# Kernel tuning notes

Hardware: AMD Instinct MI355X
Metric: run time of the kernel (lower is better)

## Reference

```python
import jax, jax.numpy as jnp
import numpy as np

EPS = 1e-7  # keras.backend.epsilon()
NUM_ROUTING = 3


def squash(v, axis=-1):
    s2 = jnp.sum(jnp.square(v), axis=axis, keepdims=True)
    scale = s2 / (1.0 + s2) / jnp.sqrt(s2 + EPS)
    return scale * v


def setup_inputs() -> dict:
    key = jax.random.key(0)
    k1, k2 = jax.random.split(key)
    B, N_in, C, d_in, d_out = 64, 4096, 10, 8, 16
    x = jax.random.normal(k1, (B, N_in, d_in), dtype=jnp.float32)
    # glorot-ish scale for transformation weights [N_in, C, d_in, d_out]
    W = jax.random.normal(k2, (N_in, C, d_in, d_out), dtype=jnp.float32) * (1.0 / np.sqrt(d_in + d_out))
    return {"x": x, "W": W}


def reference(x, W):
    # u_hat[b,n,c,e] = sum_d x[b,n,d] * W[n,c,d,e]  -- the tile+multiply+reduce in the original
    u_hat = jnp.einsum('bnd,ncde->bnce', x, W)  # [B, N_in, C, d_out]
    B, N_in, C, _ = u_hat.shape
    b = jnp.zeros((B, N_in, C), dtype=u_hat.dtype)
    v = None
    for i in range(NUM_ROUTING):
        c = jax.nn.softmax(b, axis=2)                    # [B, N_in, C]
        s = jnp.einsum('bnc,bnce->bce', c, u_hat)        # [B, C, d_out]
        v = squash(s)                                    # [B, C, d_out]
        if i < NUM_ROUTING - 1:
            agreement = jnp.einsum('bnce,bce->bnc', u_hat, v)
            b = b + agreement
    return v
```

## Files before the change

kernel.cpp:

```cpp
#include <hip/hip_runtime.h>
#include <hip/hip_fp16.h>

#define B_ 64
#define N_ 4096
#define C_ 10
#define D_ 8
#define E_ 16
#define EPS_ 1e-7f
#define NT_ 4
#define NBLK_ (N_ / NT_)
#define NSLOT_ NBLK_
#define PROW_ 80
#define NSG_ 8

typedef _Float16 h2_t __attribute__((ext_vector_type(2)));
typedef __fp16   p2_t __attribute__((ext_vector_type(2)));

__device__ inline unsigned pkh(float a, float b) {
    p2_t t = __builtin_amdgcn_cvt_pkrtz(a, b);
    return *(unsigned*)&t;
}
#if __has_builtin(__builtin_amdgcn_fdot2)
__device__ inline float fd2(unsigned a, unsigned b, float c) {
    h2_t av = *(h2_t*)&a, bv = *(h2_t*)&b;
    return __builtin_amdgcn_fdot2(av, bv, c, false);
}
#else
__device__ inline float fd2(unsigned a, unsigned b, float c) {
    h2_t av = *(h2_t*)&a, bv = *(h2_t*)&b;
    return fmaf((float)av.x, (float)bv.x, fmaf((float)av.y, (float)bv.y, c));
}
#endif
__device__ inline float hlo(unsigned u) { h2_t t = *(h2_t*)&u; return (float)t.x; }
__device__ inline float hhi(unsigned u) { h2_t t = *(h2_t*)&u; return (float)t.y; }
__device__ inline unsigned hpack(float a, float b) {
    __half2 t = __floats2half2_rn(a, b);
    return *(unsigned*)&t;
}
__device__ inline float2 hunpack(unsigned u) {
    return __half22float2(*(const __half2*)&u);
}

template <bool UNIFORM>
__global__ __launch_bounds__(256, 4) void caps_pass(
    const float* __restrict__ x, const float* __restrict__ W,
    const unsigned* __restrict__ vpk, unsigned* __restrict__ partial)
{
    __shared__ uint4    wlds[NT_ * C_ * 16];
    __shared__ unsigned xlds[NT_ * B_ * 4];
    __shared__ float    xch[2][2][2][16][2];

    const int tid = (int)threadIdx.x;
    const int blk = (int)blockIdx.x;
    const int n0  = blk * NT_;

    {
        const float4* wg = (const float4*)W + (size_t)blk * (NT_ * 320);
#pragma unroll
        for (int k = 0; k < 3; ++k) {
            const int g = k * 256 + tid;
            if (g < NT_ * C_ * 16) {
                const int n   = g / 160;
                const int rem = g - n * 160;
                const int c   = rem >> 4;
                const int r2  = rem & 15;
                const int d2  = r2 >> 2;
                const int eqs = r2 & 3;
                const float4 g0 = wg[n * 320 + c * 32 + (2 * d2) * 4 + eqs];
                const float4 g1 = wg[n * 320 + c * 32 + (2 * d2 + 1) * 4 + eqs];
                wlds[((n * C_ + c) * 4 + d2) * 4 + eqs] =
                    make_uint4(pkh(g0.x, g1.x), pkh(g0.y, g1.y),
                               pkh(g0.z, g1.z), pkh(g0.w, g1.w));
            }
        }
    }
    {
        const float4* xg = (const float4*)x;
#pragma unroll
        for (int k = 0; k < 2; ++k) {
            const int g = k * 256 + tid;
            const int b = g >> 3;
            const int r = g & 7;
            const int n = r >> 1;
            const int dq = r & 1;
            const float4 v = xg[((size_t)b * N_ + n0 + n) * 2 + dq];
            *(uint2*)&xlds[(n * B_ + b) * 4 + dq * 2] =
                make_uint2(pkh(v.x, v.y), pkh(v.z, v.w));
        }
    }
    __syncthreads();

    const int wv   = tid >> 6;
    const int lane = tid & 63;
    const int eq   = lane & 3;
    const int bl   = lane >> 2;
    const int h    = wv & 1;
    const int cg   = wv >> 1;
    const int b0   = h * 32 + bl;
    const int b1   = b0 + 16;
    const int cbase = cg * 5;

    unsigned vcp0[5][2], vcp1[5][2];
    if (!UNIFORM) {
#pragma unroll
        for (int cc = 0; cc < 5; ++cc) {
            const int c = cbase + cc;
            const uint2 a = *(const uint2*)(vpk + (b0 * C_ + c) * 8 + eq * 2);
            vcp0[cc][0] = a.x; vcp0[cc][1] = a.y;
            const uint2 d = *(const uint2*)(vpk + (b1 * C_ + c) * 8 + eq * 2);
            vcp1[cc][0] = d.x; vcp1[cc][1] = d.y;
        }
    }

    float4 acc0[5], acc1[5];
#pragma unroll
    for (int cc = 0; cc < 5; ++cc) {
        acc0[cc] = make_float4(0.f, 0.f, 0.f, 0.f);
        acc1[cc] = make_float4(0.f, 0.f, 0.f, 0.f);
    }

#pragma unroll 1
    for (int j = 0; j < NT_; ++j) {
        const uint4 xq0 = *(const uint4*)&xlds[(j * B_ + b0) * 4];
        const uint4 xq1 = *(const uint4*)&xlds[(j * B_ + b1) * 4];
        const unsigned xa[4] = {xq0.x, xq0.y, xq0.z, xq0.w};
        const unsigned xb[4] = {xq1.x, xq1.y, xq1.z, xq1.w};

        if (UNIFORM) {
#pragma unroll
            for (int cc = 0; cc < 5; ++cc) {
                const uint4* wq = &wlds[(j * C_ + cbase + cc) * 16];
#pragma unroll
                for (int d2 = 0; d2 < 4; ++d2) {
                    const uint4 q = wq[d2 * 4 + eq];
                    acc0[cc].x = fd2(xa[d2], q.x, acc0[cc].x);
                    acc0[cc].y = fd2(xa[d2], q.y, acc0[cc].y);
                    acc0[cc].z = fd2(xa[d2], q.z, acc0[cc].z);
                    acc0[cc].w = fd2(xa[d2], q.w, acc0[cc].w);
                    acc1[cc].x = fd2(xb[d2], q.x, acc1[cc].x);
                    acc1[cc].y = fd2(xb[d2], q.y, acc1[cc].y);
                    acc1[cc].z = fd2(xb[d2], q.z, acc1[cc].z);
                    acc1[cc].w = fd2(xb[d2], q.w, acc1[cc].w);
                }
            }
        } else {
            unsigned uhp0[5][2], uhp1[5][2];
            float wgt0[5], wgt1[5];
            float s0 = 0.f, s1 = 0.f;
#pragma unroll
            for (int cc = 0; cc < 5; ++cc) {
                const uint4* wq = &wlds[(j * C_ + cbase + cc) * 16];
                float4 u0 = make_float4(0.f, 0.f, 0.f, 0.f);
                float4 u1 = make_float4(0.f, 0.f, 0.f, 0.f);
#pragma unroll
                for (int d2 = 0; d2 < 4; ++d2) {
                    const uint4 q = wq[d2 * 4 + eq];
                    u0.x = fd2(xa[d2], q.x, u0.x);
                    u0.y = fd2(xa[d2], q.y, u0.y);
                    u0.z = fd2(xa[d2], q.z, u0.z);
                    u0.w = fd2(xa[d2], q.w, u0.w);
                    u1.x = fd2(xb[d2], q.x, u1.x);
                    u1.y = fd2(xb[d2], q.y, u1.y);
                    u1.z = fd2(xb[d2], q.z, u1.z);
                    u1.w = fd2(xb[d2], q.w, u1.w);
                }
                const unsigned up00 = pkh(u0.x, u0.y), up01 = pkh(u0.z, u0.w);
                const unsigned up10 = pkh(u1.x, u1.y), up11 = pkh(u1.z, u1.w);
                float t0 = fd2(up00, vcp0[cc][0], fd2(up01, vcp0[cc][1], 0.f));
                t0 += __shfl_xor(t0, 1); t0 += __shfl_xor(t0, 2);
                float t1 = fd2(up10, vcp1[cc][0], fd2(up11, vcp1[cc][1], 0.f));
                t1 += __shfl_xor(t1, 1); t1 += __shfl_xor(t1, 2);
                wgt0[cc] = __expf(t0); s0 += wgt0[cc];
                wgt1[cc] = __expf(t1); s1 += wgt1[cc];
                uhp0[cc][0] = up00; uhp0[cc][1] = up01;
                uhp1[cc][0] = up10; uhp1[cc][1] = up11;
            }
            if (eq == 0) {
                xch[j & 1][cg][h][bl][0] = s0;
                xch[j & 1][cg][h][bl][1] = s1;
            }
            __syncthreads();
            const float i0 = 1.f / (s0 + xch[j & 1][cg ^ 1][h][bl][0]);
            const float i1 = 1.f / (s1 + xch[j & 1][cg ^ 1][h][bl][1]);
#pragma unroll
            for (int cc = 0; cc < 5; ++cc) {
                const float g0 = wgt0[cc] * i0, g1 = wgt1[cc] * i1;
                acc0[cc].x = fmaf(g0, hlo(uhp0[cc][0]), acc0[cc].x);
                acc0[cc].y = fmaf(g0, hhi(uhp0[cc][0]), acc0[cc].y);
                acc0[cc].z = fmaf(g0, hlo(uhp0[cc][1]), acc0[cc].z);
                acc0[cc].w = fmaf(g0, hhi(uhp0[cc][1]), acc0[cc].w);
                acc1[cc].x = fmaf(g1, hlo(uhp1[cc][0]), acc1[cc].x);
                acc1[cc].y = fmaf(g1, hhi(uhp1[cc][0]), acc1[cc].y);
                acc1[cc].z = fmaf(g1, hlo(uhp1[cc][1]), acc1[cc].z);
                acc1[cc].w = fmaf(g1, hhi(uhp1[cc][1]), acc1[cc].w);
            }
        }
    }

    const float fold = UNIFORM ? 0.1f : 1.f;
#pragma unroll
    for (int cc = 0; cc < 5; ++cc) {
        const int c = cbase + cc;
        *(uint2*)(partial + ((size_t)b0 * NSLOT_ + blk) * PROW_ + c * 8 + eq * 2) =
            make_uint2(hpack(acc0[cc].x * fold, acc0[cc].y * fold),
                       hpack(acc0[cc].z * fold, acc0[cc].w * fold));
        *(uint2*)(partial + ((size_t)b1 * NSLOT_ + blk) * PROW_ + c * 8 + eq * 2) =
            make_uint2(hpack(acc1[cc].x * fold, acc1[cc].y * fold),
                       hpack(acc1[cc].z * fold, acc1[cc].w * fold));
    }
}

__global__ __launch_bounds__(256) void caps_redA(
    const unsigned* __restrict__ partial, float* __restrict__ sub)
{
    const int b  = (int)blockIdx.x >> 3;
    const int sg = (int)blockIdx.x & 7;
    const int tid = (int)threadIdx.x;
    const int sc   = tid >> 5;
    const int col4 = tid & 31;
    __shared__ float red[8][20][8];
    if (col4 < 20) {
        float s[8];
#pragma unroll
        for (int p = 0; p < 8; ++p) s[p] = 0.f;
        const int slot0 = sg * (NSLOT_ / NSG_) + sc * 16;
        const uint4* base = (const uint4*)(partial +
            ((size_t)b * NSLOT_ + slot0) * PROW_) + col4;
#pragma unroll 4
        for (int k = 0; k < 16; ++k) {
            const uint4 q = base[k * (PROW_ / 4)];
            const float2 f0 = hunpack(q.x), f1 = hunpack(q.y);
            const float2 f2 = hunpack(q.z), f3 = hunpack(q.w);
            s[0] += f0.x; s[1] += f0.y; s[2] += f1.x; s[3] += f1.y;
            s[4] += f2.x; s[5] += f2.y; s[6] += f3.x; s[7] += f3.y;
        }
#pragma unroll
        for (int p = 0; p < 8; ++p) red[sc][col4][p] = s[p];
    }
    __syncthreads();
    if (tid < 160) {
        const int c4 = tid >> 3, p = tid & 7;
        float s = 0.f;
#pragma unroll
        for (int ch = 0; ch < 8; ++ch) s += red[ch][c4][p];
        sub[((size_t)b * NSG_ + sg) * (C_ * E_) + c4 * 8 + p] = s;
    }
}

__global__ __launch_bounds__(128) void caps_redB(
    const float* __restrict__ sub, float* __restrict__ v_cum,
    unsigned* __restrict__ vpk, float* __restrict__ out, int mode)
{
    const int b = (int)blockIdx.x;
    const int tid = (int)threadIdx.x;
    if (tid >= PROW_) return;
    float slo = 0.f, shi = 0.f;
#pragma unroll
    for (int sg = 0; sg < NSG_; ++sg) {
        const float* p = sub + ((size_t)b * NSG_ + sg) * (C_ * E_) + tid * 2;
        slo += p[0]; shi += p[1];
    }
    float p = slo * slo + shi * shi;
    p += __shfl_xor(p, 1); p += __shfl_xor(p, 2); p += __shfl_xor(p, 4);
    const float sc = (p / (1.f + p)) * rsqrtf(p + EPS_);
    float v0 = sc * slo, v1 = sc * shi;
    const int o = b * (C_ * E_) + tid * 2;
    if (mode == 2) {
        out[o] = v0; out[o + 1] = v1;
    } else {
        if (mode == 0) {
            v_cum[o] = v0; v_cum[o + 1] = v1;
        } else {
            v0 += v_cum[o]; v1 += v_cum[o + 1];
            v_cum[o] = v0; v_cum[o + 1] = v1;
        }
        vpk[b * PROW_ + tid] = hpack(v0, v1);
    }
}

extern "C" void kernel_launch(void* const* d_in, const int* in_sizes, int n_in,
                              void* d_out, int out_size, void* d_ws, size_t ws_size,
                              hipStream_t stream) {
    const float* x = (const float*)d_in[0];
    const float* W = (const float*)d_in[1];
    float* out = (float*)d_out;

    char* p = (char*)d_ws;
    unsigned* partial = (unsigned*)p;
    p += (size_t)B_ * NSLOT_ * PROW_ * sizeof(unsigned);
    float* sub = (float*)p;
    p += (size_t)B_ * NSG_ * C_ * E_ * sizeof(float);
    float* v_cum = (float*)p;
    p += (size_t)B_ * C_ * E_ * sizeof(float);
    unsigned* vpk = (unsigned*)p;

    for (int t = 0; t < 3; ++t) {
        if (t == 0)
            caps_pass<true ><<<dim3(NBLK_), 256, 0, stream>>>(x, W, vpk, partial);
        else
            caps_pass<false><<<dim3(NBLK_), 256, 0, stream>>>(x, W, vpk, partial);
        caps_redA<<<dim3(B_ * NSG_), 256, 0, stream>>>(partial, sub);
        caps_redB<<<dim3(B_), 128, 0, stream>>>(sub, v_cum, vpk, out, t);
    }
}
```

Before: 82.87 us.

## Process eight input capsules per block with in-block pairwise reduction of partials

Doubles the capsules handled per block (NT 4→8) and uses 512 threads, so two groups of waves each take four capsules and their fp16 partial sums are combined through shared memory before one global write. This halves the partial buffer size and the number of slots the reduction kernel has to read. In exchange it adds an extra shared-memory round trip and barriers, halves the block count, and makes blocks larger, which may reduce occupancy.

```diff
diff --git a/kernel.cpp b/kernel.cpp
--- a/kernel.cpp
+++ b/kernel.cpp
@@ -7,10 +7,11 @@
 #define D_ 8
 #define E_ 16
 #define EPS_ 1e-7f
-#define NT_ 4
+#define NT_ 8
 #define NBLK_ (N_ / NT_)
 #define NSLOT_ NBLK_
 #define PROW_ 80
+#define WBROW_ 82
 #define NSG_ 8
 
 typedef _Float16 h2_t __attribute__((ext_vector_type(2)));
@@ -42,13 +43,15 @@
 }
 
 template <bool UNIFORM>
-__global__ __launch_bounds__(256, 4) void caps_pass(
+__global__ __launch_bounds__(512, 4) void caps_pass(
     const float* __restrict__ x, const float* __restrict__ W,
     const unsigned* __restrict__ vpk, unsigned* __restrict__ partial)
 {
-    __shared__ uint4    wlds[NT_ * C_ * 16];
-    __shared__ unsigned xlds[NT_ * B_ * 4];
-    __shared__ float    xch[2][2][2][16][2];
+    __shared__ __align__(16) char smem[30720];
+    uint4*    wlds = (uint4*)smem;
+    unsigned* xlds = (unsigned*)(smem + 20480);
+    float*    xch  = (float*)(smem + 28672);
+    unsigned* wb   = (unsigned*)smem;
 
     const int tid = (int)threadIdx.x;
     const int blk = (int)blockIdx.x;
@@ -58,7 +61,7 @@
         const float4* wg = (const float4*)W + (size_t)blk * (NT_ * 320);
 #pragma unroll
         for (int k = 0; k < 3; ++k) {
-            const int g = k * 256 + tid;
+            const int g = k * 512 + tid;
             if (g < NT_ * C_ * 16) {
                 const int n   = g / 160;
                 const int rem = g - n * 160;
@@ -78,9 +81,9 @@
         const float4* xg = (const float4*)x;
 #pragma unroll
         for (int k = 0; k < 2; ++k) {
-            const int g = k * 256 + tid;
-            const int b = g >> 3;
-            const int r = g & 7;
+            const int g = k * 512 + tid;
+            const int b = g >> 4;
+            const int r = g & 15;
             const int n = r >> 1;
             const int dq = r & 1;
             const float4 v = xg[((size_t)b * N_ + n0 + n) * 2 + dq];
@@ -95,10 +98,13 @@
     const int eq   = lane & 3;
     const int bl   = lane >> 2;
     const int h    = wv & 1;
-    const int cg   = wv >> 1;
+    const int cg   = (wv >> 1) & 1;
+    const int np   = wv >> 2;
     const int b0   = h * 32 + bl;
     const int b1   = b0 + 16;
     const int cbase = cg * 5;
+    float* xme = xch + (((cg) * 4 + np * 2 + h) * 16 + bl) * 2;
+    float* xot = xch + (((cg ^ 1) * 4 + np * 2 + h) * 16 + bl) * 2;
 
     unsigned vcp0[5][2], vcp1[5][2];
     if (!UNIFORM) {
@@ -120,16 +126,17 @@
     }
 
 #pragma unroll 1
-    for (int j = 0; j < NT_; ++j) {
-        const uint4 xq0 = *(const uint4*)&xlds[(j * B_ + b0) * 4];
-        const uint4 xq1 = *(const uint4*)&xlds[(j * B_ + b1) * 4];
+    for (int j = 0; j < 4; ++j) {
+        const int nl = np * 4 + j;
+        const uint4 xq0 = *(const uint4*)&xlds[(nl * B_ + b0) * 4];
+        const uint4 xq1 = *(const uint4*)&xlds[(nl * B_ + b1) * 4];
         const unsigned xa[4] = {xq0.x, xq0.y, xq0.z, xq0.w};
         const unsigned xb[4] = {xq1.x, xq1.y, xq1.z, xq1.w};
 
         if (UNIFORM) {
 #pragma unroll
             for (int cc = 0; cc < 5; ++cc) {
-                const uint4* wq = &wlds[(j * C_ + cbase + cc) * 16];
+                const uint4* wq = &wlds[(nl * C_ + cbase + cc) * 16];
 #pragma unroll
                 for (int d2 = 0; d2 < 4; ++d2) {
                     const uint4 q = wq[d2 * 4 + eq];
@@ -149,7 +156,7 @@
             float s0 = 0.f, s1 = 0.f;
 #pragma unroll
             for (int cc = 0; cc < 5; ++cc) {
-                const uint4* wq = &wlds[(j * C_ + cbase + cc) * 16];
+                const uint4* wq = &wlds[(nl * C_ + cbase + cc) * 16];
                 float4 u0 = make_float4(0.f, 0.f, 0.f, 0.f);
                 float4 u1 = make_float4(0.f, 0.f, 0.f, 0.f);
 #pragma unroll
@@ -175,13 +182,10 @@
                 uhp0[cc][0] = up00; uhp0[cc][1] = up01;
                 uhp1[cc][0] = up10; uhp1[cc][1] = up11;
             }
-            if (eq == 0) {
-                xch[j & 1][cg][h][bl][0] = s0;
-                xch[j & 1][cg][h][bl][1] = s1;
-            }
+            if (eq == 0) { xme[0] = s0; xme[1] = s1; }
             __syncthreads();
-            const float i0 = 1.f / (s0 + xch[j & 1][cg ^ 1][h][bl][0]);
-            const float i1 = 1.f / (s1 + xch[j & 1][cg ^ 1][h][bl][1]);
+            const float i0 = 1.f / (s0 + xot[0]);
+            const float i1 = 1.f / (s1 + xot[1]);
 #pragma unroll
             for (int cc = 0; cc < 5; ++cc) {
                 const float g0 = wgt0[cc] * i0, g1 = wgt1[cc] * i1;
@@ -198,15 +202,35 @@
     }
 
     const float fold = UNIFORM ? 0.1f : 1.f;
-#pragma unroll
-    for (int cc = 0; cc < 5; ++cc) {
-        const int c = cbase + cc;
-        *(uint2*)(partial + ((size_t)b0 * NSLOT_ + blk) * PROW_ + c * 8 + eq * 2) =
-            make_uint2(hpack(acc0[cc].x * fold, acc0[cc].y * fold),
-                       hpack(acc0[cc].z * fold, acc0[cc].w * fold));
-        *(uint2*)(partial + ((size_t)b1 * NSLOT_ + blk) * PROW_ + c * 8 + eq * 2) =
-            make_uint2(hpack(acc1[cc].x * fold, acc1[cc].y * fold),
-                       hpack(acc1[cc].z * fold, acc1[cc].w * fold));
+    __syncthreads();
+    if (np == 1) {
+#pragma unroll
+        for (int cc = 0; cc < 5; ++cc) {
+            const int c = cbase + cc;
+            *(uint2*)&wb[b0 * WBROW_ + c * 8 + eq * 2] =
+                make_uint2(hpack(acc0[cc].x * fold, acc0[cc].y * fold),
+                           hpack(acc0[cc].z * fold, acc0[cc].w * fold));
+            *(uint2*)&wb[b1 * WBROW_ + c * 8 + eq * 2] =
+                make_uint2(hpack(acc1[cc].x * fold, acc1[cc].y * fold),
+                           hpack(acc1[cc].z * fold, acc1[cc].w * fold));
+        }
+    }
+    __syncthreads();
+    if (np == 0) {
+#pragma unroll
+        for (int cc = 0; cc < 5; ++cc) {
+            const int c = cbase + cc;
+            const uint2 p0 = *(const uint2*)&wb[b0 * WBROW_ + c * 8 + eq * 2];
+            const float2 a0 = hunpack(p0.x), a1 = hunpack(p0.y);
+            *(uint2*)(partial + ((size_t)b0 * NSLOT_ + blk) * PROW_ + c * 8 + eq * 2) =
+                make_uint2(hpack(a0.x + acc0[cc].x * fold, a0.y + acc0[cc].y * fold),
+                           hpack(a1.x + acc0[cc].z * fold, a1.y + acc0[cc].w * fold));
+            const uint2 p1 = *(const uint2*)&wb[b1 * WBROW_ + c * 8 + eq * 2];
+            const float2 d0 = hunpack(p1.x), d1 = hunpack(p1.y);
+            *(uint2*)(partial + ((size_t)b1 * NSLOT_ + blk) * PROW_ + c * 8 + eq * 2) =
+                make_uint2(hpack(d0.x + acc1[cc].x * fold, d0.y + acc1[cc].y * fold),
+                           hpack(d1.x + acc1[cc].z * fold, d1.y + acc1[cc].w * fold));
+        }
     }
 }
 
@@ -223,11 +247,11 @@
         float s[8];
 #pragma unroll
         for (int p = 0; p < 8; ++p) s[p] = 0.f;
-        const int slot0 = sg * (NSLOT_ / NSG_) + sc * 16;
+        const int slot0 = sg * (NSLOT_ / NSG_) + sc * 8;
         const uint4* base = (const uint4*)(partial +
             ((size_t)b * NSLOT_ + slot0) * PROW_) + col4;
 #pragma unroll 4
-        for (int k = 0; k < 16; ++k) {
+        for (int k = 0; k < 8; ++k) {
             const uint4 q = base[k * (PROW_ / 4)];
             const float2 f0 = hunpack(q.x), f1 = hunpack(q.y);
             const float2 f2 = hunpack(q.z), f3 = hunpack(q.w);
@@ -296,9 +320,9 @@
 
     for (int t = 0; t < 3; ++t) {
         if (t == 0)
-            caps_pass<true ><<<dim3(NBLK_), 256, 0, stream>>>(x, W, vpk, partial);
+            caps_pass<true ><<<dim3(NBLK_), 512, 0, stream>>>(x, W, vpk, partial);
         else
-            caps_pass<false><<<dim3(NBLK_), 256, 0, stream>>>(x, W, vpk, partial);
+            caps_pass<false><<<dim3(NBLK_), 512, 0, stream>>>(x, W, vpk, partial);
         caps_redA<<<dim3(B_ * NSG_), 256, 0, stream>>>(partial, sub);
         caps_redB<<<dim3(B_), 128, 0, stream>>>(sub, v_cum, vpk, out, t);
     }
```

Result: faster. 78.12 us, median of 2 (-5.7%).
